# Performance work log

Measured on AMD Instinct MI355X. Metric: run time of the kernel, lower is better.

## Reference

```python
import jax, jax.numpy as jnp
import numpy as np


def _log_exp_kernel(x):
    # positive feature map log(1 + exp(x)) (softplus), per the kernel's name
    return jax.nn.softplus(x)


def setup_inputs() -> dict:
    key0 = jax.random.key(0)
    ks = jax.random.split(key0, 8)
    N, L, H, d = 2, 2048, 8, 64
    D = H * d
    s = 1.0 / np.sqrt(D)
    return {
        "query": jax.random.normal(ks[0], (N, L, D), jnp.float32),
        "key": jax.random.normal(ks[1], (N, L, D), jnp.float32),
        "Wq": jax.random.normal(ks[2], (D, D), jnp.float32) * s,
        "Wk": jax.random.normal(ks[3], (D, D), jnp.float32) * s,
        "Wv": jax.random.normal(ks[4], (D, D), jnp.float32) * s,
        "position_coeffs": jax.random.normal(ks[5], (H, d), jnp.float32),
        "position_weight": jax.random.normal(ks[6], (H, d, 1), jnp.float32) * 0.02,
        "position_bias": jax.random.normal(ks[7], (H, d), jnp.float32) * 0.02,
    }


def reference(query, key, Wq, Wk, Wv, position_coeffs, position_weight, position_bias):
    N, Lq, D = query.shape
    Lk = key.shape[1]
    H, d, P = position_weight.shape

    # default positions: arange, P=1 (broadcast over batch)
    qpos = jnp.arange(Lq, dtype=query.dtype).reshape(1, Lq, 1)  # (1, Lq, P)

    # projections + kernel feature map; (N, H, L, d)
    q = _log_exp_kernel((query @ Wq.T).reshape(N, Lq, H, d)).transpose(0, 2, 1, 3)
    k = _log_exp_kernel((key @ Wk.T).reshape(N, Lk, H, d)).transpose(0, 2, 1, 3)
    v = (key @ Wv.T).reshape(N, Lk, H, d).transpose(0, 2, 1, 3)

    # projected positions; NOTE: source uses query_positions for pk too (faithful)
    pq = jnp.einsum('nlp,hkp->nhlk', qpos, position_weight) + position_bias[None, :, None, :]
    pk = jnp.einsum('nlp,hkp->nhlk', qpos, position_weight)  # (1, H, Lq, d)

    coeff = position_coeffs[None, :, None, :]  # (1, H, 1, d)
    cos_a = q * jnp.cos(pq)
    cos_b = coeff * k * jnp.cos(pk)
    sin_a = q * jnp.sin(pq)
    sin_b = coeff * k * jnp.sin(pk)

    # (N, H, Lq, Lk) quadratic score
    score = (jnp.einsum('nhqd,nhkd->nhqk', cos_a, cos_b)
             + jnp.einsum('nhqd,nhkd->nhqk', sin_a, sin_b))

    # future mask (future_offset = 0): zero out keys j > query i
    future = jnp.arange(Lk)[None, :] > jnp.arange(Lq)[:, None]
    score = jnp.where(future[None, None], jnp.zeros((), score.dtype), score)

    # scaled: rows sum (in abs) to 1
    score = score / jnp.sum(jnp.abs(score), axis=-1, keepdims=True)

    att = jnp.einsum('nhqk,nhkd->nhqd', score, v)
    return att.transpose(0, 2, 1, 3).reshape(N, Lq, D)
```

## Files before the change

### kernel.cpp

```cpp
#include <hip/hip_runtime.h>
#include <hip/hip_bf16.h>
#include <cstdint>


typedef __bf16 bf16x8 __attribute__((ext_vector_type(8)));
typedef float f32x16 __attribute__((ext_vector_type(16)));
typedef unsigned short u16x8 __attribute__((ext_vector_type(8)));

__device__ __forceinline__ unsigned short f2bfu(float f) {
    uint32_t u = __float_as_uint(f);
    uint32_t r = (u + 0x7fffu + ((u >> 16) & 1u)) >> 16;
    return (unsigned short)r;
}
__device__ __forceinline__ uint32_t cvt2(float a, float b) {
    __hip_bfloat162 h = __float22bfloat162_rn(make_float2(a, b));
    return *reinterpret_cast<uint32_t*>(&h);
}
__device__ __forceinline__ float softplusf(float x) {
    return fmaxf(x, 0.f) + __logf(1.f + __expf(-fabsf(x)));
}

__global__ __launch_bounds__(256) void proj_kernel(
    const float* __restrict__ query, const float* __restrict__ key,
    const float* __restrict__ Wq, const float* __restrict__ Wk,
    const float* __restrict__ Wv, const float* __restrict__ coef,
    const float* __restrict__ posw, const float* __restrict__ posb,
    unsigned short* __restrict__ Af, unsigned short* __restrict__ Bf,
    unsigned short* __restrict__ Vf)
{
    const int mode = blockIdx.z;
    const int c0 = blockIdx.x * 128;
    const int m0 = blockIdx.y * 64;
    const float* X = (mode == 0) ? query : key;
    const float* W = (mode == 0) ? Wq : (mode == 1 ? Wk : Wv);

    __shared__ __align__(16) char smem[64 * 72 * 2 + 128 * 72 * 2];
    unsigned short* Xs = (unsigned short*)smem;
    unsigned short* Ws = (unsigned short*)(smem + 64 * 72 * 2);

    const int t = threadIdx.x;
    const int lane = t & 63, wv = t >> 6;
    const int lm = lane & 31, half = lane >> 5;
    const int wrow = wv >> 1, wcol = wv & 1;

    f32x16 acc[2] = {};

    float4 px[4], pw[8];
    {
#pragma unroll
        for (int it = 0; it < 4; ++it) {
            int cid = t + it * 256, row = cid >> 4, off = (cid & 15) << 2;
            px[it] = *(const float4*)&X[(size_t)(m0 + row) * 512 + off];
        }
#pragma unroll
        for (int it = 0; it < 8; ++it) {
            int cid = t + it * 256, row = cid >> 4, off = (cid & 15) << 2;
            pw[it] = *(const float4*)&W[(size_t)(c0 + row) * 512 + off];
        }
    }

    for (int kt = 0; kt < 8; ++kt) {
        __syncthreads();
#pragma unroll
        for (int it = 0; it < 4; ++it) {
            int cid = t + it * 256, row = cid >> 4, off = (cid & 15) << 2;
            uint2 p = { cvt2(px[it].x, px[it].y), cvt2(px[it].z, px[it].w) };
            *(uint2*)&Xs[row * 72 + off] = p;
        }
#pragma unroll
        for (int it = 0; it < 8; ++it) {
            int cid = t + it * 256, row = cid >> 4, off = (cid & 15) << 2;
            uint2 p = { cvt2(pw[it].x, pw[it].y), cvt2(pw[it].z, pw[it].w) };
            *(uint2*)&Ws[row * 72 + off] = p;
        }
        __syncthreads();
        if (kt < 7) {
            int ko = (kt + 1) * 64;
#pragma unroll
            for (int it = 0; it < 4; ++it) {
                int cid = t + it * 256, row = cid >> 4, off = (cid & 15) << 2;
                px[it] = *(const float4*)&X[(size_t)(m0 + row) * 512 + ko + off];
            }
#pragma unroll
            for (int it = 0; it < 8; ++it) {
                int cid = t + it * 256, row = cid >> 4, off = (cid & 15) << 2;
                pw[it] = *(const float4*)&W[(size_t)(c0 + row) * 512 + ko + off];
            }
        }
        const unsigned short* ab = &Xs[(32 * wrow + lm) * 72 + half * 8];
        const unsigned short* bb = &Ws[(64 * wcol + lm) * 72 + half * 8];
#pragma unroll
        for (int ks = 0; ks < 4; ++ks) {
            bf16x8 a  = *(const bf16x8*)(ab + ks * 16);
            bf16x8 b0 = *(const bf16x8*)(bb + ks * 16);
            bf16x8 b1 = *(const bf16x8*)(bb + 32 * 72 + ks * 16);
            acc[0] = __builtin_amdgcn_mfma_f32_32x32x16_bf16(a, b0, acc[0], 0, 0, 0);
            acc[1] = __builtin_amdgcn_mfma_f32_32x32x16_bf16(a, b1, acc[1], 0, 0, 0);
        }
    }

    if (mode != 2) {
        unsigned short* Feat = (mode == 0) ? Af : Bf;
#pragma unroll
        for (int j = 0; j < 2; ++j)
#pragma unroll
        for (int r = 0; r < 16; ++r) {
            int rl = (r & 3) + 8 * (r >> 2) + 4 * half;
            int m = m0 + 32 * wrow + rl;
            int c = c0 + 64 * wcol + 32 * j + lm;
            int n = m >> 11, l = m & 2047;
            int h = c >> 6, jj = c & 63;
            float ang = (float)l * posw[c] + ((mode == 0) ? posb[c] : 0.f);
            float sn, cs; __sincosf(ang, &sn, &cs);
            float v = softplusf(acc[j][r]);
            if (mode == 1) v *= coef[c];
            size_t base = ((size_t)(n * 8 + h) * 2048 + l) * 128 + jj;
            Feat[base]      = f2bfu(v * cs);
            Feat[base + 64] = f2bfu(v * sn);
        }
    } else {
        float* tb = (float*)smem;
        float* tbw = tb + wv * (32 * 34);
        __syncthreads();
#pragma unroll
        for (int j = 0; j < 2; ++j) {
            __syncthreads();
#pragma unroll
            for (int r = 0; r < 16; ++r) {
                int rl = (r & 3) + 8 * (r >> 2) + 4 * half;
                tbw[lm * 34 + rl] = acc[j][r];
            }
            __syncthreads();
            int mb = m0 + 32 * wrow;
            int n = mb >> 11, l0 = mb & 2047;
#pragma unroll
            for (int rep = 0; rep < 16; ++rep) {
                int cl = rep * 2 + half;
                float v = tbw[cl * 34 + lm];
                int c = c0 + 64 * wcol + 32 * j + cl;
                int h = c >> 6, dd = c & 63;
                Vf[((size_t)(n * 8 + h) * 64 + dd) * 2048 + l0 + lm] = f2bfu(v);
            }
        }
    }
}

__global__ __launch_bounds__(256) void attn_kernel(
    const unsigned short* __restrict__ Af, const unsigned short* __restrict__ Bf,
    const unsigned short* __restrict__ Vf, float* __restrict__ out)
{
    const int bx = blockIdx.x;
    const int nh = bx & 15;
    const int p  = bx >> 4;
    const int qq = (p < 16) ? p : 47 - p;
    const int q0 = qq * 64;

    __shared__ unsigned short Bs[64 * 136];
    __shared__ unsigned short Ss[64 * 72];
    __shared__ unsigned short Vs[64 * 72];
    __shared__ float zf[64];

    const int t = threadIdx.x;
    const int lane = t & 63, wv = t >> 6;
    const int lm = lane & 31, half = lane >> 5;
    const int wrow = wv >> 1, wcol = wv & 1;
    const int n = nh >> 3, h = nh & 7;

    const unsigned short* Ah = Af + (size_t)nh * 2048 * 128;
    const unsigned short* Bh = Bf + (size_t)nh * 2048 * 128;
    const unsigned short* Vh = Vf + (size_t)nh * 64 * 2048;

#pragma unroll
    for (int it = 0; it < 4; ++it) {
        int cid = t + it * 256, row = cid >> 4, off = (cid & 15) << 3;
        *(u16x8*)&Bs[row * 136 + off] = *(const u16x8*)&Ah[(size_t)(q0 + row) * 128 + off];
    }
    if (t < 64) zf[t] = 0.f;
    __syncthreads();
    bf16x8 afrag[8];
    {
        const unsigned short* ab = &Bs[(32 * wrow + lm) * 136 + half * 8];
#pragma unroll
        for (int c = 0; c < 8; ++c) afrag[c] = *(const bf16x8*)(ab + c * 16);
    }

    f32x16 oacc = {};
    float zp[16];
#pragma unroll
    for (int r = 0; r < 16; ++r) zp[r] = 0.f;

    u16x8 pb[4], pv[2];
#pragma unroll
    for (int it = 0; it < 4; ++it) {
        int cid = t + it * 256, row = cid >> 4, off = (cid & 15) << 3;
        pb[it] = *(const u16x8*)&Bh[(size_t)row * 128 + off];
    }
#pragma unroll
    for (int it = 0; it < 2; ++it) {
        int cid = t + it * 256, row = cid >> 3, off = (cid & 7) << 3;
        pv[it] = *(const u16x8*)&Vh[(size_t)row * 2048 + off];
    }

    for (int kt = 0; kt <= qq; ++kt) {
        __syncthreads();
#pragma unroll
        for (int it = 0; it < 4; ++it) {
            int cid = t + it * 256, row = cid >> 4, off = (cid & 15) << 3;
            *(u16x8*)&Bs[row * 136 + off] = pb[it];
        }
#pragma unroll
        for (int it = 0; it < 2; ++it) {
            int cid = t + it * 256, row = cid >> 3, off = (cid & 7) << 3;
            *(u16x8*)&Vs[row * 72 + off] = pv[it];
        }
        __syncthreads();
        if (kt < qq) {
            int k1 = (kt + 1) * 64;
#pragma unroll
            for (int it = 0; it < 4; ++it) {
                int cid = t + it * 256, row = cid >> 4, off = (cid & 15) << 3;
                pb[it] = *(const u16x8*)&Bh[(size_t)(k1 + row) * 128 + off];
            }
#pragma unroll
            for (int it = 0; it < 2; ++it) {
                int cid = t + it * 256, row = cid >> 3, off = (cid & 7) << 3;
                pv[it] = *(const u16x8*)&Vh[(size_t)row * 2048 + k1 + off];
            }
        }

        f32x16 sacc = {};
        const unsigned short* bbase = &Bs[(32 * wcol + lm) * 136 + half * 8];
#pragma unroll
        for (int ks = 0; ks < 8; ++ks) {
            bf16x8 b = *(const bf16x8*)(bbase + ks * 16);
            sacc = __builtin_amdgcn_mfma_f32_32x32x16_bf16(afrag[ks], b, sacc, 0, 0, 0);
        }
        if (kt == qq) {
#pragma unroll
            for (int r = 0; r < 16; ++r) {
                int rl = (r & 3) + 8 * (r >> 2) + 4 * half;
                if ((32 * wcol + lm) > (32 * wrow + rl)) sacc[r] = 0.f;
            }
        }
#pragma unroll
        for (int r = 0; r < 16; ++r) zp[r] += fabsf(sacc[r]);

#pragma unroll
        for (int r = 0; r < 16; ++r) {
            int rl = (r & 3) + 8 * (r >> 2) + 4 * half;
            Ss[(32 * wrow + rl) * 72 + 32 * wcol + lm] = f2bfu(sacc[r]);
        }
        __syncthreads();

        const unsigned short* sbase = &Ss[(32 * wrow + lm) * 72 + half * 8];
        const unsigned short* vbase = &Vs[(32 * wcol + lm) * 72 + half * 8];
#pragma unroll
        for (int kc = 0; kc < 4; ++kc) {
            bf16x8 a = *(const bf16x8*)(sbase + kc * 16);
            bf16x8 b = *(const bf16x8*)(vbase + kc * 16);
            oacc = __builtin_amdgcn_mfma_f32_32x32x16_bf16(a, b, oacc, 0, 0, 0);
        }
    }

    __syncthreads();
#pragma unroll
    for (int r = 0; r < 16; ++r) {
        float z = zp[r];
        z += __shfl_xor(z, 1);
        z += __shfl_xor(z, 2);
        z += __shfl_xor(z, 4);
        z += __shfl_xor(z, 8);
        z += __shfl_xor(z, 16);
        if (lm == 0) {
            int rl = (r & 3) + 8 * (r >> 2) + 4 * half;
            atomicAdd(&zf[32 * wrow + rl], z);
        }
    }
    __syncthreads();
#pragma unroll
    for (int r = 0; r < 16; ++r) {
        int rl = (r & 3) + 8 * (r >> 2) + 4 * half;
        int q = q0 + 32 * wrow + rl;
        float invz = 1.f / zf[32 * wrow + rl];
        out[((size_t)(n * 2048 + q)) * 512 + h * 64 + 32 * wcol + lm] = oacc[r] * invz;
    }
}

extern "C" void kernel_launch(void* const* d_in, const int* in_sizes, int n_in,
                              void* d_out, int out_size, void* d_ws, size_t ws_size,
                              hipStream_t stream) {
    (void)in_sizes; (void)n_in; (void)out_size; (void)ws_size;
    const float* query = (const float*)d_in[0];
    const float* key   = (const float*)d_in[1];
    const float* Wq    = (const float*)d_in[2];
    const float* Wk    = (const float*)d_in[3];
    const float* Wv    = (const float*)d_in[4];
    const float* coef  = (const float*)d_in[5];
    const float* posw  = (const float*)d_in[6];
    const float* posb  = (const float*)d_in[7];

    unsigned short* Af = (unsigned short*)d_ws;
    unsigned short* Bf = Af + (size_t)16 * 2048 * 128;
    unsigned short* Vf = Bf + (size_t)16 * 2048 * 128;

    proj_kernel<<<dim3(4, 64, 3), 256, 0, stream>>>(
        query, key, Wq, Wk, Wv, coef, posw, posb, Af, Bf, Vf);
    attn_kernel<<<dim3(512), 256, 0, stream>>>(
        Af, Bf, Vf, (float*)d_out);
}
```

Before: 138.8 us.

## Split attention key loop across two blocks by parity and combine in a normalize kernel

Each query tile's key-block loop is now split between two thread blocks (even and odd key tiles), doubling the grid to 1024 blocks. Each block writes an unnormalized partial output and a partial row-abs-sum, and a new norm kernel adds the partials and divides. The change also splits the QK MFMA chain into two accumulators, adds s_setprio around the MFMA sections and sets launch_bounds occupancy to 4. It is meant to improve load balance and occupancy on the causal triangle, at the cost of an extra kernel launch and extra global traffic for the partial output.

```diff
diff --git a/kernel.cpp b/kernel.cpp
--- a/kernel.cpp
+++ b/kernel.cpp
@@ -145,11 +145,14 @@
     }
 }
 
-__global__ __launch_bounds__(256) void attn_kernel(
+__global__ __launch_bounds__(256, 4) void attn_kernel(
     const unsigned short* __restrict__ Af, const unsigned short* __restrict__ Bf,
-    const unsigned short* __restrict__ Vf, float* __restrict__ out)
+    const unsigned short* __restrict__ Vf, float* __restrict__ out,
+    float* __restrict__ opart, float* __restrict__ z0, float* __restrict__ z1)
 {
-    const int bx = blockIdx.x;
+    const int bid = blockIdx.x;
+    const int parity = bid >> 9;
+    const int bx = bid & 511;
     const int nh = bx & 15;
     const int p  = bx >> 4;
     const int qq = (p < 16) ? p : 47 - p;
@@ -190,18 +193,21 @@
     for (int r = 0; r < 16; ++r) zp[r] = 0.f;
 
     u16x8 pb[4], pv[2];
-#pragma unroll
-    for (int it = 0; it < 4; ++it) {
-        int cid = t + it * 256, row = cid >> 4, off = (cid & 15) << 3;
-        pb[it] = *(const u16x8*)&Bh[(size_t)row * 128 + off];
-    }
-#pragma unroll
-    for (int it = 0; it < 2; ++it) {
-        int cid = t + it * 256, row = cid >> 3, off = (cid & 7) << 3;
-        pv[it] = *(const u16x8*)&Vh[(size_t)row * 2048 + off];
-    }
-
-    for (int kt = 0; kt <= qq; ++kt) {
+    {
+        const int kbase = parity * 64;
+#pragma unroll
+        for (int it = 0; it < 4; ++it) {
+            int cid = t + it * 256, row = cid >> 4, off = (cid & 15) << 3;
+            pb[it] = *(const u16x8*)&Bh[(size_t)(kbase + row) * 128 + off];
+        }
+#pragma unroll
+        for (int it = 0; it < 2; ++it) {
+            int cid = t + it * 256, row = cid >> 3, off = (cid & 7) << 3;
+            pv[it] = *(const u16x8*)&Vh[(size_t)row * 2048 + kbase + off];
+        }
+    }
+
+    for (int kt = parity; kt <= qq; kt += 2) {
         __syncthreads();
 #pragma unroll
         for (int it = 0; it < 4; ++it) {
@@ -214,8 +220,8 @@
             *(u16x8*)&Vs[row * 72 + off] = pv[it];
         }
         __syncthreads();
-        if (kt < qq) {
-            int k1 = (kt + 1) * 64;
+        if (kt + 2 <= qq) {
+            int k1 = (kt + 2) * 64;
 #pragma unroll
             for (int it = 0; it < 4; ++it) {
                 int cid = t + it * 256, row = cid >> 4, off = (cid & 15) << 3;
@@ -228,13 +234,20 @@
             }
         }
 
-        f32x16 sacc = {};
+        f32x16 sacc = {}, sacc1 = {};
         const unsigned short* bbase = &Bs[(32 * wcol + lm) * 136 + half * 8];
-#pragma unroll
-        for (int ks = 0; ks < 8; ++ks) {
-            bf16x8 b = *(const bf16x8*)(bbase + ks * 16);
-            sacc = __builtin_amdgcn_mfma_f32_32x32x16_bf16(afrag[ks], b, sacc, 0, 0, 0);
-        }
+        __builtin_amdgcn_s_setprio(1);
+#pragma unroll
+        for (int ks = 0; ks < 8; ks += 2) {
+            bf16x8 b0 = *(const bf16x8*)(bbase + ks * 16);
+            bf16x8 b1 = *(const bf16x8*)(bbase + (ks + 1) * 16);
+            sacc  = __builtin_amdgcn_mfma_f32_32x32x16_bf16(afrag[ks],     b0, sacc,  0, 0, 0);
+            sacc1 = __builtin_amdgcn_mfma_f32_32x32x16_bf16(afrag[ks + 1], b1, sacc1, 0, 0, 0);
+        }
+        __builtin_amdgcn_s_setprio(0);
+#pragma unroll
+        for (int r = 0; r < 16; ++r) sacc[r] += sacc1[r];
+
         if (kt == qq) {
 #pragma unroll
             for (int r = 0; r < 16; ++r) {
@@ -254,12 +267,14 @@
 
         const unsigned short* sbase = &Ss[(32 * wrow + lm) * 72 + half * 8];
         const unsigned short* vbase = &Vs[(32 * wcol + lm) * 72 + half * 8];
+        __builtin_amdgcn_s_setprio(1);
 #pragma unroll
         for (int kc = 0; kc < 4; ++kc) {
             bf16x8 a = *(const bf16x8*)(sbase + kc * 16);
             bf16x8 b = *(const bf16x8*)(vbase + kc * 16);
             oacc = __builtin_amdgcn_mfma_f32_32x32x16_bf16(a, b, oacc, 0, 0, 0);
         }
+        __builtin_amdgcn_s_setprio(0);
     }
 
     __syncthreads();
@@ -277,13 +292,39 @@
         }
     }
     __syncthreads();
+
+    float* zdst = parity ? z1 : z0;
+    if (t < 64) zdst[(size_t)nh * 2048 + q0 + t] = zf[t];
+
+    float* dst = parity ? opart : out;
 #pragma unroll
     for (int r = 0; r < 16; ++r) {
         int rl = (r & 3) + 8 * (r >> 2) + 4 * half;
         int q = q0 + 32 * wrow + rl;
-        float invz = 1.f / zf[32 * wrow + rl];
-        out[((size_t)(n * 2048 + q)) * 512 + h * 64 + 32 * wcol + lm] = oacc[r] * invz;
-    }
+        dst[((size_t)(n * 2048 + q)) * 512 + h * 64 + 32 * wcol + lm] = oacc[r];
+    }
+}
+
+__global__ __launch_bounds__(256) void norm_kernel(
+    const float* __restrict__ opart, const float* __restrict__ z0,
+    const float* __restrict__ z1, float* __restrict__ out)
+{
+    int idx = blockIdx.x * 256 + threadIdx.x;
+    int i = idx << 2;
+    int row = i >> 9;
+    int c = i & 511;
+    int n = row >> 11, q = row & 2047;
+    int h = c >> 6;
+    size_t zi = (size_t)(n * 8 + h) * 2048 + q;
+    float rz = 1.f / (z0[zi] + z1[zi]);
+    float4 o = *(const float4*)&out[i];
+    float4 pp = *(const float4*)&opart[i];
+    float4 r;
+    r.x = (o.x + pp.x) * rz;
+    r.y = (o.y + pp.y) * rz;
+    r.z = (o.z + pp.z) * rz;
+    r.w = (o.w + pp.w) * rz;
+    *(float4*)&out[i] = r;
 }
 
 extern "C" void kernel_launch(void* const* d_in, const int* in_sizes, int n_in,
@@ -302,9 +343,14 @@
     unsigned short* Af = (unsigned short*)d_ws;
     unsigned short* Bf = Af + (size_t)16 * 2048 * 128;
     unsigned short* Vf = Bf + (size_t)16 * 2048 * 128;
+    float* opart = (float*)(Vf + (size_t)16 * 64 * 2048);
+    float* z0    = opart + (size_t)2 * 2048 * 512;
+    float* z1    = z0 + (size_t)16 * 2048;
 
     proj_kernel<<<dim3(4, 64, 3), 256, 0, stream>>>(
         query, key, Wq, Wk, Wv, coef, posw, posb, Af, Bf, Vf);
-    attn_kernel<<<dim3(512), 256, 0, stream>>>(
-        Af, Bf, Vf, (float*)d_out);
-}
+    attn_kernel<<<dim3(1024), 256, 0, stream>>>(
+        Af, Bf, Vf, (float*)d_out, opart, z0, z1);
+    norm_kernel<<<dim3(2048), 256, 0, stream>>>(
+        opart, z0, z1, (float*)d_out);
+}
```

Measured after the change: 214.1 us. 54.3% more time.

## Pre-convert inputs to bf16, enlarge projection tiles, add MFMA priority hints

Applied to the files above, without the earlier changes.

Adds a separate conversion kernel that turns the fp32 inputs and weights into bf16 once, so the projection GEMM loads half the bytes and does no per-tile conversion. The projection tile grows from 64x128 to 128x128, with each wave computing a 2x2 grid of 32x32 MFMA tiles, which doubles operand reuse and halves the grid. It also wraps the MFMA loops in both kernels with s_setprio. The cost is an extra launch plus a write and re-read of bf16 copies through the workspace. The V transpose path also drops its inner __syncthreads, which looks safe only because each wave uses its own staging region.

```diff
diff --git a/kernel.cpp b/kernel.cpp
--- a/kernel.cpp
+++ b/kernel.cpp
@@ -20,42 +20,65 @@
     return fmaxf(x, 0.f) + __logf(1.f + __expf(-fabsf(x)));
 }
 
-__global__ __launch_bounds__(256) void proj_kernel(
+__global__ __launch_bounds__(256) void cvt_kernel(
     const float* __restrict__ query, const float* __restrict__ key,
     const float* __restrict__ Wq, const float* __restrict__ Wk,
-    const float* __restrict__ Wv, const float* __restrict__ coef,
+    const float* __restrict__ Wv,
+    unsigned short* __restrict__ Xqb, unsigned short* __restrict__ Xkb,
+    unsigned short* __restrict__ Wqb, unsigned short* __restrict__ Wkb,
+    unsigned short* __restrict__ Wvb)
+{
+    const int z = blockIdx.z;
+    const float* src;
+    unsigned short* dst;
+    int n8;
+    if (z == 0)      { src = query; dst = Xqb; n8 = 4096 * 512 / 8; }
+    else if (z == 1) { src = key;   dst = Xkb; n8 = 4096 * 512 / 8; }
+    else if (z == 2) { src = Wq;    dst = Wqb; n8 = 512 * 512 / 8;  }
+    else if (z == 3) { src = Wk;    dst = Wkb; n8 = 512 * 512 / 8;  }
+    else             { src = Wv;    dst = Wvb; n8 = 512 * 512 / 8;  }
+    int idx = blockIdx.x * 256 + threadIdx.x;
+    if (idx >= n8) return;
+    const float4* s = (const float4*)src + (size_t)idx * 2;
+    float4 a = s[0], b = s[1];
+    uint4 o;
+    o.x = cvt2(a.x, a.y); o.y = cvt2(a.z, a.w);
+    o.z = cvt2(b.x, b.y); o.w = cvt2(b.z, b.w);
+    *(uint4*)&dst[(size_t)idx * 8] = o;
+}
+
+__global__ __launch_bounds__(256) void proj_kernel(
+    const unsigned short* __restrict__ Xqb, const unsigned short* __restrict__ Xkb,
+    const unsigned short* __restrict__ Wqb, const unsigned short* __restrict__ Wkb,
+    const unsigned short* __restrict__ Wvb, const float* __restrict__ coef,
     const float* __restrict__ posw, const float* __restrict__ posb,
     unsigned short* __restrict__ Af, unsigned short* __restrict__ Bf,
     unsigned short* __restrict__ Vf)
 {
     const int mode = blockIdx.z;
     const int c0 = blockIdx.x * 128;
-    const int m0 = blockIdx.y * 64;
-    const float* X = (mode == 0) ? query : key;
-    const float* W = (mode == 0) ? Wq : (mode == 1 ? Wk : Wv);
-
-    __shared__ __align__(16) char smem[64 * 72 * 2 + 128 * 72 * 2];
+    const int m0 = blockIdx.y * 128;
+    const unsigned short* X = (mode == 0) ? Xqb : Xkb;
+    const unsigned short* W = (mode == 0) ? Wqb : (mode == 1 ? Wkb : Wvb);
+
+    __shared__ __align__(16) char smem[128 * 72 * 2 * 2];
     unsigned short* Xs = (unsigned short*)smem;
-    unsigned short* Ws = (unsigned short*)(smem + 64 * 72 * 2);
+    unsigned short* Ws = (unsigned short*)(smem + 128 * 72 * 2);
 
     const int t = threadIdx.x;
     const int lane = t & 63, wv = t >> 6;
     const int lm = lane & 31, half = lane >> 5;
     const int wrow = wv >> 1, wcol = wv & 1;
 
-    f32x16 acc[2] = {};
-
-    float4 px[4], pw[8];
+    f32x16 acc[2][2] = {};
+
+    u16x8 px[4], pw[4];
     {
 #pragma unroll
         for (int it = 0; it < 4; ++it) {
-            int cid = t + it * 256, row = cid >> 4, off = (cid & 15) << 2;
-            px[it] = *(const float4*)&X[(size_t)(m0 + row) * 512 + off];
-        }
-#pragma unroll
-        for (int it = 0; it < 8; ++it) {
-            int cid = t + it * 256, row = cid >> 4, off = (cid & 15) << 2;
-            pw[it] = *(const float4*)&W[(size_t)(c0 + row) * 512 + off];
+            int cid = t + it * 256, row = cid >> 3, seg = cid & 7;
+            px[it] = *(const u16x8*)&X[(size_t)(m0 + row) * 512 + seg * 8];
+            pw[it] = *(const u16x8*)&W[(size_t)(c0 + row) * 512 + seg * 8];
         }
     }
 
@@ -63,56 +86,53 @@
         __syncthreads();
 #pragma unroll
         for (int it = 0; it < 4; ++it) {
-            int cid = t + it * 256, row = cid >> 4, off = (cid & 15) << 2;
-            uint2 p = { cvt2(px[it].x, px[it].y), cvt2(px[it].z, px[it].w) };
-            *(uint2*)&Xs[row * 72 + off] = p;
-        }
-#pragma unroll
-        for (int it = 0; it < 8; ++it) {
-            int cid = t + it * 256, row = cid >> 4, off = (cid & 15) << 2;
-            uint2 p = { cvt2(pw[it].x, pw[it].y), cvt2(pw[it].z, pw[it].w) };
-            *(uint2*)&Ws[row * 72 + off] = p;
+            int cid = t + it * 256, row = cid >> 3, seg = cid & 7;
+            *(u16x8*)&Xs[row * 72 + seg * 8] = px[it];
+            *(u16x8*)&Ws[row * 72 + seg * 8] = pw[it];
         }
         __syncthreads();
         if (kt < 7) {
             int ko = (kt + 1) * 64;
 #pragma unroll
             for (int it = 0; it < 4; ++it) {
-                int cid = t + it * 256, row = cid >> 4, off = (cid & 15) << 2;
-                px[it] = *(const float4*)&X[(size_t)(m0 + row) * 512 + ko + off];
-            }
-#pragma unroll
-            for (int it = 0; it < 8; ++it) {
-                int cid = t + it * 256, row = cid >> 4, off = (cid & 15) << 2;
-                pw[it] = *(const float4*)&W[(size_t)(c0 + row) * 512 + ko + off];
-            }
-        }
-        const unsigned short* ab = &Xs[(32 * wrow + lm) * 72 + half * 8];
+                int cid = t + it * 256, row = cid >> 3, seg = cid & 7;
+                px[it] = *(const u16x8*)&X[(size_t)(m0 + row) * 512 + ko + seg * 8];
+                pw[it] = *(const u16x8*)&W[(size_t)(c0 + row) * 512 + ko + seg * 8];
+            }
+        }
+        const unsigned short* ab = &Xs[(64 * wrow + lm) * 72 + half * 8];
         const unsigned short* bb = &Ws[(64 * wcol + lm) * 72 + half * 8];
+        __builtin_amdgcn_s_setprio(1);
 #pragma unroll
         for (int ks = 0; ks < 4; ++ks) {
-            bf16x8 a  = *(const bf16x8*)(ab + ks * 16);
+            bf16x8 a0 = *(const bf16x8*)(ab + ks * 16);
+            bf16x8 a1 = *(const bf16x8*)(ab + 32 * 72 + ks * 16);
             bf16x8 b0 = *(const bf16x8*)(bb + ks * 16);
             bf16x8 b1 = *(const bf16x8*)(bb + 32 * 72 + ks * 16);
-            acc[0] = __builtin_amdgcn_mfma_f32_32x32x16_bf16(a, b0, acc[0], 0, 0, 0);
-            acc[1] = __builtin_amdgcn_mfma_f32_32x32x16_bf16(a, b1, acc[1], 0, 0, 0);
-        }
+            acc[0][0] = __builtin_amdgcn_mfma_f32_32x32x16_bf16(a0, b0, acc[0][0], 0, 0, 0);
+            acc[0][1] = __builtin_amdgcn_mfma_f32_32x32x16_bf16(a0, b1, acc[0][1], 0, 0, 0);
+            acc[1][0] = __builtin_amdgcn_mfma_f32_32x32x16_bf16(a1, b0, acc[1][0], 0, 0, 0);
+            acc[1][1] = __builtin_amdgcn_mfma_f32_32x32x16_bf16(a1, b1, acc[1][1], 0, 0, 0);
+        }
+        __builtin_amdgcn_s_setprio(0);
     }
 
     if (mode != 2) {
         unsigned short* Feat = (mode == 0) ? Af : Bf;
 #pragma unroll
+        for (int i = 0; i < 2; ++i)
+#pragma unroll
         for (int j = 0; j < 2; ++j)
 #pragma unroll
         for (int r = 0; r < 16; ++r) {
             int rl = (r & 3) + 8 * (r >> 2) + 4 * half;
-            int m = m0 + 32 * wrow + rl;
+            int m = m0 + 64 * wrow + 32 * i + rl;
             int c = c0 + 64 * wcol + 32 * j + lm;
             int n = m >> 11, l = m & 2047;
             int h = c >> 6, jj = c & 63;
             float ang = (float)l * posw[c] + ((mode == 0) ? posb[c] : 0.f);
             float sn, cs; __sincosf(ang, &sn, &cs);
-            float v = softplusf(acc[j][r]);
+            float v = softplusf(acc[i][j][r]);
             if (mode == 1) v *= coef[c];
             size_t base = ((size_t)(n * 8 + h) * 2048 + l) * 128 + jj;
             Feat[base]      = f2bfu(v * cs);
@@ -123,15 +143,15 @@
         float* tbw = tb + wv * (32 * 34);
         __syncthreads();
 #pragma unroll
+        for (int i = 0; i < 2; ++i)
+#pragma unroll
         for (int j = 0; j < 2; ++j) {
-            __syncthreads();
 #pragma unroll
             for (int r = 0; r < 16; ++r) {
                 int rl = (r & 3) + 8 * (r >> 2) + 4 * half;
-                tbw[lm * 34 + rl] = acc[j][r];
-            }
-            __syncthreads();
-            int mb = m0 + 32 * wrow;
+                tbw[lm * 34 + rl] = acc[i][j][r];
+            }
+            int mb = m0 + 64 * wrow + 32 * i;
             int n = mb >> 11, l0 = mb & 2047;
 #pragma unroll
             for (int rep = 0; rep < 16; ++rep) {
@@ -230,11 +250,13 @@
 
         f32x16 sacc = {};
         const unsigned short* bbase = &Bs[(32 * wcol + lm) * 136 + half * 8];
+        __builtin_amdgcn_s_setprio(1);
 #pragma unroll
         for (int ks = 0; ks < 8; ++ks) {
             bf16x8 b = *(const bf16x8*)(bbase + ks * 16);
             sacc = __builtin_amdgcn_mfma_f32_32x32x16_bf16(afrag[ks], b, sacc, 0, 0, 0);
         }
+        __builtin_amdgcn_s_setprio(0);
         if (kt == qq) {
 #pragma unroll
             for (int r = 0; r < 16; ++r) {
@@ -254,12 +276,14 @@
 
         const unsigned short* sbase = &Ss[(32 * wrow + lm) * 72 + half * 8];
         const unsigned short* vbase = &Vs[(32 * wcol + lm) * 72 + half * 8];
+        __builtin_amdgcn_s_setprio(1);
 #pragma unroll
         for (int kc = 0; kc < 4; ++kc) {
             bf16x8 a = *(const bf16x8*)(sbase + kc * 16);
             bf16x8 b = *(const bf16x8*)(vbase + kc * 16);
             oacc = __builtin_amdgcn_mfma_f32_32x32x16_bf16(a, b, oacc, 0, 0, 0);
         }
+        __builtin_amdgcn_s_setprio(0);
     }
 
     __syncthreads();
@@ -299,12 +323,19 @@
     const float* posw  = (const float*)d_in[6];
     const float* posb  = (const float*)d_in[7];
 
-    unsigned short* Af = (unsigned short*)d_ws;
-    unsigned short* Bf = Af + (size_t)16 * 2048 * 128;
-    unsigned short* Vf = Bf + (size_t)16 * 2048 * 128;
-
-    proj_kernel<<<dim3(4, 64, 3), 256, 0, stream>>>(
-        query, key, Wq, Wk, Wv, coef, posw, posb, Af, Bf, Vf);
+    unsigned short* Af  = (unsigned short*)d_ws;
+    unsigned short* Bf  = Af + (size_t)16 * 2048 * 128;
+    unsigned short* Vf  = Bf + (size_t)16 * 2048 * 128;
+    unsigned short* Xqb = Vf + (size_t)16 * 64 * 2048;
+    unsigned short* Xkb = Xqb + (size_t)4096 * 512;
+    unsigned short* Wqb = Xkb + (size_t)4096 * 512;
+    unsigned short* Wkb = Wqb + (size_t)512 * 512;
+    unsigned short* Wvb = Wkb + (size_t)512 * 512;
+
+    cvt_kernel<<<dim3(1024, 1, 5), 256, 0, stream>>>(
+        query, key, Wq, Wk, Wv, Xqb, Xkb, Wqb, Wkb, Wvb);
+    proj_kernel<<<dim3(4, 32, 3), 256, 0, stream>>>(
+        Xqb, Xkb, Wqb, Wkb, Wvb, coef, posw, posb, Af, Bf, Vf);
     attn_kernel<<<dim3(512), 256, 0, stream>>>(
         Af, Bf, Vf, (float*)d_out);
 }
```

Result: slower. 143.0 us (+3.1%).
